# Kernel optimization log

Measured on AMD Instinct MI355X. Metric: run time of the kernel, lower is better.

Reference implementation:

```python
import jax, jax.numpy as jnp
import numpy as np
from jax import lax

B, C, H, W = 32, 3, 256, 256
P, D, E, K = 16, 256, 8, 2
HP, WP = H // P, W // P
N = HP * WP
GATE_IN = C * P * P  # 768
GATE_HID = D // 2    # 128


def _mk(key, shape, scale=0.02):
    return scale * jax.random.normal(key, shape, dtype=jnp.float32)


def setup_inputs() -> dict:
    key = jax.random.key(0)
    ks = jax.random.split(key, 20)
    inp = {
        "x": jax.random.normal(ks[0], (B, C, H, W), dtype=jnp.float32),
        # gate MLP: Linear(768,128) -> ReLU -> Linear(128,8)
        "g_w1": _mk(ks[1], (GATE_HID, GATE_IN)),
        "g_b1": jnp.zeros((GATE_HID,), jnp.float32),
        "g_w2": _mk(ks[2], (E, GATE_HID)),
        "g_b2": jnp.zeros((E,), jnp.float32),
        # per-expert CNN params, stacked with leading expert dim E
        "dw1_w": _mk(ks[3], (E, 3, 1, 3, 3)),   "dw1_b": jnp.zeros((E, 3), jnp.float32),
        "pw1_w": _mk(ks[4], (E, 64, 3, 1, 1)),  "pw1_b": jnp.zeros((E, 64), jnp.float32),
        "dw2_w": _mk(ks[5], (E, 64, 1, 3, 3)),  "dw2_b": jnp.zeros((E, 64), jnp.float32),
        "pw2_w": _mk(ks[6], (E, 128, 64, 1, 1)), "pw2_b": jnp.zeros((E, 128), jnp.float32),
        "dw3_w": _mk(ks[7], (E, 128, 1, 3, 3)), "dw3_b": jnp.zeros((E, 128), jnp.float32),
        "pw3_w": _mk(ks[8], (E, D, 128, 1, 1)), "pw3_b": jnp.zeros((E, D), jnp.float32),
    }
    return inp


def _dwconv(x, w, b, stride):
    # depthwise 3x3, padding 1; x: [n, c, h, w]; w: [c, 1, 3, 3]
    c = x.shape[1]
    y = lax.conv_general_dilated(
        x, w, (stride, stride), ((1, 1), (1, 1)),
        dimension_numbers=("NCHW", "OIHW", "NCHW"), feature_group_count=c)
    return jax.nn.relu(y + b[None, :, None, None])


def _pwconv(x, w, b):
    # pointwise 1x1 conv as GEMM; w: [o, c, 1, 1]
    y = jnp.einsum("nchw,oc->nohw", x, w[:, :, 0, 0]) + b[None, :, None, None]
    return jax.nn.relu(y)


def _expert(x, dw1w, dw1b, pw1w, pw1b, dw2w, dw2b, pw2w, pw2b, dw3w, dw3b, pw3w, pw3b):
    # x: [BN, 3, 16, 16] -> [BN, D]
    x = _pwconv(_dwconv(x, dw1w, dw1b, 2), pw1w, pw1b)   # [BN, 64, 8, 8]
    x = _pwconv(_dwconv(x, dw2w, dw2b, 2), pw2w, pw2b)   # [BN, 128, 4, 4]
    x = _pwconv(_dwconv(x, dw3w, dw3b, 2), pw3w, pw3b)   # [BN, 256, 2, 2]
    return x.mean(axis=(2, 3))                            # adaptive avg pool to 1x1


def reference(x, g_w1, g_b1, g_w2, g_b2,
              dw1_w, dw1_b, pw1_w, pw1_b, dw2_w, dw2_b, pw2_w, pw2_b,
              dw3_w, dw3_b, pw3_w, pw3_b):
    b = x.shape[0]
    # nn.Unfold(kernel=P, stride=P): columns ordered (c, di, dj)
    patches = x.reshape(b, C, HP, P, WP, P).transpose(0, 2, 4, 1, 3, 5)  # [B,hp,wp,C,P,P]
    patches_sp = patches.reshape(b * N, C, P, P)
    patches_flat = patches_sp.reshape(b * N, GATE_IN)

    # gate (eval mode: dropout is identity)
    h = jax.nn.relu(patches_flat @ g_w1.T + g_b1)
    logits = h @ g_w2.T + g_b2                       # [BN, E]
    topk_vals, topk_idx = lax.top_k(logits, K)       # [BN, K]
    weights = jax.nn.softmax(topk_vals, axis=-1)
    one_hot = jax.nn.one_hot(topk_idx, E, dtype=x.dtype)   # [BN, K, E]
    routing = (one_hot * weights[..., None]).sum(axis=1)   # [BN, E]

    # run all experts densely (as the original does), then combine
    expert_outs = jax.vmap(_expert, in_axes=(None,) + (0,) * 12)(
        patches_sp, dw1_w, dw1_b, pw1_w, pw1_b, dw2_w, dw2_b,
        pw2_w, pw2_b, dw3_w, dw3_b, pw3_w, pw3_b)   # [E, BN, D]
    out = jnp.einsum("ne,end->nd", routing, expert_outs)  # [BN, D]

    features = out.reshape(b, HP, WP, D).transpose(0, 3, 1, 2)  # [B, D, hp, wp]
    load_balance_loss = jnp.float32(0.0)  # eval mode
    return features, load_balance_loss
```

## Files before the change

### kernel.cpp

```cpp
#include <hip/hip_runtime.h>

#define BN 8192
#define GIN 768

#define O_ROUTE_I 0UL
#define O_ROUTE_W (O_ROUTE_I + (size_t)BN*2*4)
#define O_COUNTS  (O_ROUTE_W + (size_t)BN*2*4)
#define O_LISTS   (O_COUNTS + 256)
#define O_PW2T    (O_LISTS + (size_t)8*BN*4)
#define O_PW3T    (O_PW2T + (size_t)8*64*128*4)
#define O_SLOT    (O_PW3T + (size_t)8*128*256*4)

__global__ __launch_bounds__(256) void k0_prep(const float* __restrict__ pw2w,
                                               const float* __restrict__ pw3w,
                                               float* __restrict__ pw2t,
                                               float* __restrict__ pw3t,
                                               int* __restrict__ counts)
{
    int tid = blockIdx.x * 256 + threadIdx.x;
    if (tid < 8) counts[tid] = 0;
    for (int idx = tid; idx < 8 * 128 * 64; idx += 256 * 256) {
        int e = idx >> 13; int r = idx & 8191; int oc = r >> 6; int c = r & 63;
        pw2t[(size_t)e * 8192 + c * 128 + oc] = pw2w[idx];
    }
    for (int idx = tid; idx < 8 * 256 * 128; idx += 256 * 256) {
        int e = idx >> 15; int r = idx & 32767; int oc = r >> 7; int c = r & 127;
        pw3t[(size_t)e * 32768 + c * 256 + oc] = pw3w[idx];
    }
}

__global__ __launch_bounds__(256) void k1_gate(
    const float* __restrict__ x, const float* __restrict__ w1,
    const float* __restrict__ b1, const float* __restrict__ w2,
    const float* __restrict__ b2,
    int* __restrict__ route_i, float* __restrict__ route_w,
    int* __restrict__ counts, int* __restrict__ lists)
{
    __shared__ __align__(16) float A[32][44];
    __shared__ __align__(16) float Wl[32][132];
    __shared__ float hl[32][132];
    __shared__ float ll[32][8];

    int tid = threadIdx.x;
    int pblk = blockIdx.x * 32;

    int pgrp = tid & 7;
    int hgrp = tid >> 3;
    float acc[4][4] = {};

    int sp  = tid >> 3;
    int sk4 = (tid & 7) * 4;
    int swh = tid >> 1;
    int swk = (tid & 1) * 16;

    int patchA = pblk + sp;
    int bA = patchA >> 8; int nA = patchA & 255; int hpA = nA >> 4; int wpA = nA & 15;

    for (int kc = 0; kc < GIN; kc += 32) {
        {
            int k = kc + sk4;
            int c = k >> 8; int rem = k & 255; int ri = rem >> 4; int j = rem & 15;
            const float* src = x + (((size_t)(bA * 3 + c) * 256 + hpA * 16 + ri) * 256 + wpA * 16 + j);
            float4 a4 = *reinterpret_cast<const float4*>(src);
            A[sk4 + 0][sp] = a4.x; A[sk4 + 1][sp] = a4.y;
            A[sk4 + 2][sp] = a4.z; A[sk4 + 3][sp] = a4.w;
        }
        {
            const float* wsrc = w1 + (size_t)swh * GIN + kc + swk;
            #pragma unroll
            for (int q = 0; q < 4; q++) {
                float4 w4 = *reinterpret_cast<const float4*>(wsrc + q * 4);
                Wl[swk + q * 4 + 0][swh] = w4.x; Wl[swk + q * 4 + 1][swh] = w4.y;
                Wl[swk + q * 4 + 2][swh] = w4.z; Wl[swk + q * 4 + 3][swh] = w4.w;
            }
        }
        __syncthreads();
        float cacc[4][4] = {};
        #pragma unroll
        for (int k2 = 0; k2 < 32; k2++) {
            float4 av = *reinterpret_cast<const float4*>(&A[k2][pgrp * 4]);
            float4 wv = *reinterpret_cast<const float4*>(&Wl[k2][hgrp * 4]);
            float aa[4] = {av.x, av.y, av.z, av.w};
            float ww[4] = {wv.x, wv.y, wv.z, wv.w};
            #pragma unroll
            for (int i = 0; i < 4; i++) {
                #pragma unroll
                for (int jj = 0; jj < 4; jj++) cacc[i][jj] += aa[i] * ww[jj];
            }
        }
        #pragma unroll
        for (int i = 0; i < 4; i++) {
            #pragma unroll
            for (int jj = 0; jj < 4; jj++) acc[i][jj] += cacc[i][jj];
        }
        __syncthreads();
    }

    #pragma unroll
    for (int jj = 0; jj < 4; jj++) {
        float bb = b1[hgrp * 4 + jj];
        #pragma unroll
        for (int i = 0; i < 4; i++) {
            float v = acc[i][jj] + bb;
            hl[pgrp * 4 + i][hgrp * 4 + jj] = v > 0.f ? v : 0.f;
        }
    }
    __syncthreads();

    {
        int lp = tid >> 3; int le = tid & 7;
        float lacc = b2[le];
        const float* wrow = w2 + le * 128;
        for (int h = 0; h < 128; h++) lacc += hl[lp][h] * wrow[h];
        ll[lp][le] = lacc;
    }
    __syncthreads();

    if (tid < 32) {
        int patch = pblk + tid;
        float v[8];
        #pragma unroll
        for (int e = 0; e < 8; e++) v[e] = ll[tid][e];
        int e0 = 0; float m0 = v[0];
        #pragma unroll
        for (int e = 1; e < 8; e++) if (v[e] > m0) { m0 = v[e]; e0 = e; }
        int e1 = -1; float m1 = -3.0e38f;
        #pragma unroll
        for (int e = 0; e < 8; e++) if (e != e0 && v[e] > m1) { m1 = v[e]; e1 = e; }
        float t = expf(m1 - m0);
        float w0 = 1.f / (1.f + t);
        float w1v = t * w0;
        route_i[patch * 2] = e0; route_i[patch * 2 + 1] = e1;
        route_w[patch * 2] = w0; route_w[patch * 2 + 1] = w1v;
        int p0 = atomicAdd(&counts[e0], 1);
        lists[e0 * BN + p0] = patch * 2;
        int p1 = atomicAdd(&counts[e1], 1);
        lists[e1 * BN + p1] = patch * 2 + 1;
    }
}

__global__ __launch_bounds__(256, 3) void k23_expert(
    const float* __restrict__ x, const int* __restrict__ counts,
    const int* __restrict__ lists,
    const float* __restrict__ dw1w, const float* __restrict__ dw1b,
    const float* __restrict__ pw1w, const float* __restrict__ pw1b,
    const float* __restrict__ dw2w, const float* __restrict__ dw2b,
    const float* __restrict__ pw2t, const float* __restrict__ pw2b,
    const float* __restrict__ dw3w, const float* __restrict__ dw3b,
    const float* __restrict__ pw3t, const float* __restrict__ pw3b,
    float* __restrict__ slot)
{
    __shared__ __align__(16) float buf1[4][2176];
    __shared__ __align__(16) float buf2[4][1088];
    __shared__ int psl[4];

    int e = blockIdx.x & 7;
    int chunk = blockIdx.x >> 3;
    int cnt = counts[e];
    int base = chunk * 4;
    if (base >= cnt) return;
    int n_en = cnt - base; if (n_en > 4) n_en = 4;
    int tid = threadIdx.x;
    if (tid < 4) psl[tid] = (tid < n_en) ? lists[e * BN + base + tid] : 0;
    __syncthreads();

    int en = tid >> 6; int l = tid & 63;
    bool act = en < n_en;
    int pslot = psl[en];
    int patch = pslot >> 1;
    int b = patch >> 8, nn = patch & 255, hp = nn >> 4, wp = nn & 15;

    float* pl  = buf1[en];
    float* d1  = buf1[en] + 1024;
    float* p2  = buf1[en];
    float* d2t = buf2[en];
    float* d3  = buf2[en];

    if (act) {
        int r = l >> 2; int j4 = (l & 3) * 4;
        #pragma unroll
        for (int c = 0; c < 3; c++) {
            const float* src = x + (((size_t)(b * 3 + c) * 256 + hp * 16 + r) * 256 + wp * 16 + j4);
            float4 v = *reinterpret_cast<const float4*>(src);
            *reinterpret_cast<float4*>(&pl[c * 320 + r * 20 + j4]) = v;
        }
    }
    __syncthreads();

    if (act) {
        int oh = l >> 3, ow = l & 7;
        #pragma unroll
        for (int c = 0; c < 3; c++) {
            const float* w9 = dw1w + (e * 3 + c) * 9;
            float acc = dw1b[e * 3 + c];
            #pragma unroll
            for (int ki = 0; ki < 3; ki++) {
                int ih = oh * 2 - 1 + ki;
                if ((unsigned)ih < 16u) {
                    #pragma unroll
                    for (int kj = 0; kj < 3; kj++) {
                        int iw = ow * 2 - 1 + kj;
                        if ((unsigned)iw < 16u) acc += pl[c * 320 + ih * 20 + iw] * w9[ki * 3 + kj];
                    }
                }
            }
            d1[c * 64 + l] = acc > 0.f ? acc : 0.f;
        }
    }
    __syncthreads();

    if (act) {
        const float* w3 = pw1w + (e * 64 + l) * 3;
        float pw0 = w3[0], pw1v = w3[1], pw2v = w3[2];
        float pb = pw1b[e * 64 + l];
        float p1r[64];
        #pragma unroll
        for (int p4 = 0; p4 < 16; p4++) {
            float4 a0 = *reinterpret_cast<const float4*>(&d1[0 * 64 + p4 * 4]);
            float4 a1 = *reinterpret_cast<const float4*>(&d1[1 * 64 + p4 * 4]);
            float4 a2 = *reinterpret_cast<const float4*>(&d1[2 * 64 + p4 * 4]);
            float v0 = pb + a0.x * pw0 + a1.x * pw1v + a2.x * pw2v;
            float v1 = pb + a0.y * pw0 + a1.y * pw1v + a2.y * pw2v;
            float v2 = pb + a0.z * pw0 + a1.z * pw1v + a2.z * pw2v;
            float v3 = pb + a0.w * pw0 + a1.w * pw1v + a2.w * pw2v;
            p1r[p4 * 4 + 0] = v0 > 0.f ? v0 : 0.f;
            p1r[p4 * 4 + 1] = v1 > 0.f ? v1 : 0.f;
            p1r[p4 * 4 + 2] = v2 > 0.f ? v2 : 0.f;
            p1r[p4 * 4 + 3] = v3 > 0.f ? v3 : 0.f;
        }
        const float* w9 = dw2w + (e * 64 + l) * 9;
        float wd[9];
        #pragma unroll
        for (int i = 0; i < 9; i++) wd[i] = w9[i];
        float bd = dw2b[e * 64 + l];
        #pragma unroll
        for (int pos = 0; pos < 16; pos++) {
            int oh = pos >> 2, ow = pos & 3;
            float acc = bd;
            #pragma unroll
            for (int ki = 0; ki < 3; ki++) {
                int ih = oh * 2 - 1 + ki;
                if ((unsigned)ih < 8u) {
                    #pragma unroll
                    for (int kj = 0; kj < 3; kj++) {
                        int iw = ow * 2 - 1 + kj;
                        if ((unsigned)iw < 8u) acc += p1r[ih * 8 + iw] * wd[ki * 3 + kj];
                    }
                }
            }
            d2t[pos * 68 + l] = acc > 0.f ? acc : 0.f;
        }
    }
    __syncthreads();

    {
        int ocg = l & 15; int pq = l >> 4;
        int oc0 = ocg * 8; int p0 = pq * 4;
        if (act) {
            float acc[8][4] = {};
            const float* wbase = pw2t + (size_t)e * 8192;
            for (int c4 = 0; c4 < 16; c4++) {
                float4 a0 = *reinterpret_cast<const float4*>(&d2t[(p0 + 0) * 68 + c4 * 4]);
                float4 a1 = *reinterpret_cast<const float4*>(&d2t[(p0 + 1) * 68 + c4 * 4]);
                float4 a2 = *reinterpret_cast<const float4*>(&d2t[(p0 + 2) * 68 + c4 * 4]);
                float4 a3 = *reinterpret_cast<const float4*>(&d2t[(p0 + 3) * 68 + c4 * 4]);
                float av[4][4] = {{a0.x, a1.x, a2.x, a3.x}, {a0.y, a1.y, a2.y, a3.y},
                                  {a0.z, a1.z, a2.z, a3.z}, {a0.w, a1.w, a2.w, a3.w}};
                #pragma unroll
                for (int cc = 0; cc < 4; cc++) {
                    int c = c4 * 4 + cc;
                    float4 wa = *reinterpret_cast<const float4*>(wbase + c * 128 + oc0);
                    float4 wb = *reinterpret_cast<const float4*>(wbase + c * 128 + oc0 + 4);
                    float wv[8] = {wa.x, wa.y, wa.z, wa.w, wb.x, wb.y, wb.z, wb.w};
                    #pragma unroll
                    for (int j = 0; j < 8; j++) {
                        #pragma unroll
                        for (int i = 0; i < 4; i++) acc[j][i] += wv[j] * av[cc][i];
                    }
                }
            }
            #pragma unroll
            for (int j = 0; j < 8; j++) {
                float bb = pw2b[e * 128 + oc0 + j];
                #pragma unroll
                for (int i = 0; i < 4; i++) {
                    float v = acc[j][i] + bb;
                    p2[(oc0 + j) * 17 + p0 + i] = v > 0.f ? v : 0.f;
                }
            }
        }
    }
    __syncthreads();

    if (act) {
        #pragma unroll
        for (int chb = 0; chb < 128; chb += 64) {
            int ch = chb + l;
            const float* w9 = dw3w + (e * 128 + ch) * 9;
            float bb = dw3b[e * 128 + ch];
            #pragma unroll
            for (int pos = 0; pos < 4; pos++) {
                int oh = pos >> 1, ow = pos & 1;
                float acc = bb;
                #pragma unroll
                for (int ki = 0; ki < 3; ki++) {
                    int ih = oh * 2 - 1 + ki;
                    if ((unsigned)ih < 4u) {
                        #pragma unroll
                        for (int kj = 0; kj < 3; kj++) {
                            int iw = ow * 2 - 1 + kj;
                            if ((unsigned)iw < 4u) acc += p2[ch * 17 + ih * 4 + iw] * w9[ki * 3 + kj];
                        }
                    }
                }
                d3[ch * 4 + pos] = acc > 0.f ? acc : 0.f;
            }
        }
    }
    __syncthreads();

    if (act) {
        int oc0 = l * 4;
        const float* wbase = pw3t + (size_t)e * 32768;
        float acc[4][4] = {};
        for (int c = 0; c < 128; c++) {
            float4 a = *reinterpret_cast<const float4*>(&d3[c * 4]);
            float4 w = *reinterpret_cast<const float4*>(wbase + c * 256 + oc0);
            float av[4] = {a.x, a.y, a.z, a.w};
            float wv[4] = {w.x, w.y, w.z, w.w};
            #pragma unroll
            for (int j = 0; j < 4; j++) {
                #pragma unroll
                for (int i = 0; i < 4; i++) acc[j][i] += wv[j] * av[i];
            }
        }
        float o4[4];
        #pragma unroll
        for (int j = 0; j < 4; j++) {
            float bb = pw3b[e * 256 + oc0 + j];
            float s = 0.f;
            #pragma unroll
            for (int i = 0; i < 4; i++) {
                float v = acc[j][i] + bb;
                s += (v > 0.f ? v : 0.f);
            }
            o4[j] = 0.25f * s;
        }
        *reinterpret_cast<float4*>(slot + (size_t)pslot * 256 + oc0) =
            make_float4(o4[0], o4[1], o4[2], o4[3]);
    }
}

__global__ __launch_bounds__(256) void k4_comb(
    const float* __restrict__ slot, const float* __restrict__ route_w,
    float* __restrict__ out)
{
    __shared__ float cl[16][257];
    int bx = blockIdx.x;
    int b = bx >> 4; int hp = bx & 15;
    int tid = threadIdx.x;
    int d = tid;
    for (int wp = 0; wp < 16; wp++) {
        int n = (b * 16 + hp) * 16 + wp;
        float w0 = route_w[n * 2], w1 = route_w[n * 2 + 1];
        float v = w0 * slot[(size_t)(n * 2) * 256 + d] + w1 * slot[(size_t)(n * 2 + 1) * 256 + d];
        cl[wp][d] = v;
    }
    __syncthreads();
    int wp = tid & 15; int dg = tid >> 4;
    for (int r = 0; r < 16; r++) {
        int dd = r * 16 + dg;
        out[(((size_t)b * 256 + dd) * 16 + hp) * 16 + wp] = cl[wp][dd];
    }
    if (bx == 0 && tid == 0) out[(size_t)BN * 256] = 0.0f;
}

extern "C" void kernel_launch(void* const* d_in, const int* in_sizes, int n_in,
                              void* d_out, int out_size, void* d_ws, size_t ws_size,
                              hipStream_t stream)
{
    const float* x    = (const float*)d_in[0];
    const float* gw1  = (const float*)d_in[1];
    const float* gb1  = (const float*)d_in[2];
    const float* gw2  = (const float*)d_in[3];
    const float* gb2  = (const float*)d_in[4];
    const float* dw1w = (const float*)d_in[5];
    const float* dw1b = (const float*)d_in[6];
    const float* pw1w = (const float*)d_in[7];
    const float* pw1b = (const float*)d_in[8];
    const float* dw2w = (const float*)d_in[9];
    const float* dw2b = (const float*)d_in[10];
    const float* pw2w = (const float*)d_in[11];
    const float* pw2b = (const float*)d_in[12];
    const float* dw3w = (const float*)d_in[13];
    const float* dw3b = (const float*)d_in[14];
    const float* pw3w = (const float*)d_in[15];
    const float* pw3b = (const float*)d_in[16];

    char* ws = (char*)d_ws;
    int*   route_i = (int*)(ws + O_ROUTE_I);
    float* route_w = (float*)(ws + O_ROUTE_W);
    int*   counts  = (int*)(ws + O_COUNTS);
    int*   lists   = (int*)(ws + O_LISTS);
    float* pw2t    = (float*)(ws + O_PW2T);
    float* pw3t    = (float*)(ws + O_PW3T);
    float* slot    = (float*)(ws + O_SLOT);
    float* out     = (float*)d_out;

    hipLaunchKernelGGL(k0_prep, dim3(256), dim3(256), 0, stream,
                       pw2w, pw3w, pw2t, pw3t, counts);
    hipLaunchKernelGGL(k1_gate, dim3(BN / 32), dim3(256), 0, stream,
                       x, gw1, gb1, gw2, gb2, route_i, route_w, counts, lists);
    hipLaunchKernelGGL(k23_expert, dim3(8 * 2048), dim3(256), 0, stream,
                       x, counts, lists, dw1w, dw1b, pw1w, pw1b, dw2w, dw2b,
                       pw2t, pw2b, dw3w, dw3b, pw3t, pw3b, slot);
    hipLaunchKernelGGL(k4_comb, dim3(512), dim3(256), 0, stream,
                       slot, route_w, out);
}
```

Measured before the change: 550.0 us.

## Make expert kernel wave-synchronous, shrink LDS, swizzle pw2 output layout

Each 64-lane wave already owns one routed patch, so every block-wide __syncthreads is removed. Inactive waves now exit early instead of being masked, and the patch slot is read straight from the list rather than staged through shared memory. The two shared buffers merge into one smaller per-wave buffer with re-planned aliasing, and launch bounds rise from 3 to 4 blocks per SM. The pw2 output drops its 17-float row padding for a 16-stride XOR-style rotated layout to avoid bank conflicts. This relies on implicit wave-level ordering of LDS accesses with no barrier or fence, which the compiler does not guarantee.

Measured after the change: 578.6 us. 5.2% more time.

```diff
diff --git a/kernel.cpp b/kernel.cpp
--- a/kernel.cpp
+++ b/kernel.cpp
@@ -139,7 +139,7 @@
     }
 }
 
-__global__ __launch_bounds__(256, 3) void k23_expert(
+__global__ __launch_bounds__(256, 4) void k23_expert(
     const float* __restrict__ x, const int* __restrict__ counts,
     const int* __restrict__ lists,
     const float* __restrict__ dw1w, const float* __restrict__ dw1b,
@@ -150,33 +150,27 @@
     const float* __restrict__ pw3t, const float* __restrict__ pw3b,
     float* __restrict__ slot)
 {
-    __shared__ __align__(16) float buf1[4][2176];
-    __shared__ __align__(16) float buf2[4][1088];
-    __shared__ int psl[4];
+    __shared__ __align__(16) float buf[4][2560];
 
     int e = blockIdx.x & 7;
     int chunk = blockIdx.x >> 3;
     int cnt = counts[e];
     int base = chunk * 4;
     if (base >= cnt) return;
-    int n_en = cnt - base; if (n_en > 4) n_en = 4;
     int tid = threadIdx.x;
-    if (tid < 4) psl[tid] = (tid < n_en) ? lists[e * BN + base + tid] : 0;
-    __syncthreads();
-
     int en = tid >> 6; int l = tid & 63;
-    bool act = en < n_en;
-    int pslot = psl[en];
+    if (base + en >= cnt) return;
+    int pslot = lists[e * BN + base + en];
     int patch = pslot >> 1;
     int b = patch >> 8, nn = patch & 255, hp = nn >> 4, wp = nn & 15;
 
-    float* pl  = buf1[en];
-    float* d1  = buf1[en] + 1024;
-    float* p2  = buf1[en];
-    float* d2t = buf2[en];
-    float* d3  = buf2[en];
-
-    if (act) {
+    float* pl  = buf[en];
+    float* d1  = buf[en] + 2048;
+    float* d2t = buf[en];
+    float* p2  = buf[en];
+    float* d3  = buf[en] + 2048;
+
+    {
         int r = l >> 2; int j4 = (l & 3) * 4;
         #pragma unroll
         for (int c = 0; c < 3; c++) {
@@ -185,9 +179,8 @@
             *reinterpret_cast<float4*>(&pl[c * 320 + r * 20 + j4]) = v;
         }
     }
-    __syncthreads();
-
-    if (act) {
+
+    {
         int oh = l >> 3, ow = l & 7;
         #pragma unroll
         for (int c = 0; c < 3; c++) {
@@ -207,9 +200,8 @@
             d1[c * 64 + l] = acc > 0.f ? acc : 0.f;
         }
     }
-    __syncthreads();
-
-    if (act) {
+
+    {
         const float* w3 = pw1w + (e * 64 + l) * 3;
         float pw0 = w3[0], pw1v = w3[1], pw2v = w3[2];
         float pb = pw1b[e * 64 + l];
@@ -251,51 +243,48 @@
             d2t[pos * 68 + l] = acc > 0.f ? acc : 0.f;
         }
     }
-    __syncthreads();
 
     {
         int ocg = l & 15; int pq = l >> 4;
         int oc0 = ocg * 8; int p0 = pq * 4;
-        if (act) {
-            float acc[8][4] = {};
-            const float* wbase = pw2t + (size_t)e * 8192;
-            for (int c4 = 0; c4 < 16; c4++) {
-                float4 a0 = *reinterpret_cast<const float4*>(&d2t[(p0 + 0) * 68 + c4 * 4]);
-                float4 a1 = *reinterpret_cast<const float4*>(&d2t[(p0 + 1) * 68 + c4 * 4]);
-                float4 a2 = *reinterpret_cast<const float4*>(&d2t[(p0 + 2) * 68 + c4 * 4]);
-                float4 a3 = *reinterpret_cast<const float4*>(&d2t[(p0 + 3) * 68 + c4 * 4]);
-                float av[4][4] = {{a0.x, a1.x, a2.x, a3.x}, {a0.y, a1.y, a2.y, a3.y},
-                                  {a0.z, a1.z, a2.z, a3.z}, {a0.w, a1.w, a2.w, a3.w}};
+        float acc[8][4] = {};
+        const float* wbase = pw2t + (size_t)e * 8192;
+        for (int c4 = 0; c4 < 16; c4++) {
+            float4 a0 = *reinterpret_cast<const float4*>(&d2t[(p0 + 0) * 68 + c4 * 4]);
+            float4 a1 = *reinterpret_cast<const float4*>(&d2t[(p0 + 1) * 68 + c4 * 4]);
+            float4 a2 = *reinterpret_cast<const float4*>(&d2t[(p0 + 2) * 68 + c4 * 4]);
+            float4 a3 = *reinterpret_cast<const float4*>(&d2t[(p0 + 3) * 68 + c4 * 4]);
+            float av[4][4] = {{a0.x, a1.x, a2.x, a3.x}, {a0.y, a1.y, a2.y, a3.y},
+                              {a0.z, a1.z, a2.z, a3.z}, {a0.w, a1.w, a2.w, a3.w}};
+            #pragma unroll
+            for (int cc = 0; cc < 4; cc++) {
+                int c = c4 * 4 + cc;
+                float4 wa = *reinterpret_cast<const float4*>(wbase + c * 128 + oc0);
+                float4 wb = *reinterpret_cast<const float4*>(wbase + c * 128 + oc0 + 4);
+                float wv[8] = {wa.x, wa.y, wa.z, wa.w, wb.x, wb.y, wb.z, wb.w};
                 #pragma unroll
-                for (int cc = 0; cc < 4; cc++) {
-                    int c = c4 * 4 + cc;
-                    float4 wa = *reinterpret_cast<const float4*>(wbase + c * 128 + oc0);
-                    float4 wb = *reinterpret_cast<const float4*>(wbase + c * 128 + oc0 + 4);
-                    float wv[8] = {wa.x, wa.y, wa.z, wa.w, wb.x, wb.y, wb.z, wb.w};
+                for (int j = 0; j < 8; j++) {
                     #pragma unroll
-                    for (int j = 0; j < 8; j++) {
-                        #pragma unroll
-                        for (int i = 0; i < 4; i++) acc[j][i] += wv[j] * av[cc][i];
-                    }
+                    for (int i = 0; i < 4; i++) acc[j][i] += wv[j] * av[cc][i];
                 }
             }
-            #pragma unroll
-            for (int j = 0; j < 8; j++) {
-                float bb = pw2b[e * 128 + oc0 + j];
-                #pragma unroll
-                for (int i = 0; i < 4; i++) {
-                    float v = acc[j][i] + bb;
-                    p2[(oc0 + j) * 17 + p0 + i] = v > 0.f ? v : 0.f;
-                }
-            }
-        }
-    }
-    __syncthreads();
-
-    if (act) {
+        }
+        #pragma unroll
+        for (int j = 0; j < 8; j++) {
+            float bb = pw2b[e * 128 + oc0 + j];
+            #pragma unroll
+            for (int i = 0; i < 4; i++) {
+                float v = acc[j][i] + bb;
+                p2[(oc0 + j) * 16 + ((p0 + i + ocg) & 15)] = v > 0.f ? v : 0.f;
+            }
+        }
+    }
+
+    {
         #pragma unroll
         for (int chb = 0; chb < 128; chb += 64) {
             int ch = chb + l;
+            int grp = ch >> 3;
             const float* w9 = dw3w + (e * 128 + ch) * 9;
             float bb = dw3b[e * 128 + ch];
             #pragma unroll
@@ -309,7 +298,8 @@
                         #pragma unroll
                         for (int kj = 0; kj < 3; kj++) {
                             int iw = ow * 2 - 1 + kj;
-                            if ((unsigned)iw < 4u) acc += p2[ch * 17 + ih * 4 + iw] * w9[ki * 3 + kj];
+                            if ((unsigned)iw < 4u)
+                                acc += p2[ch * 16 + ((ih * 4 + iw + grp) & 15)] * w9[ki * 3 + kj];
                         }
                     }
                 }
@@ -317,9 +307,8 @@
             }
         }
     }
-    __syncthreads();
-
-    if (act) {
+
+    {
         int oc0 = l * 4;
         const float* wbase = pw3t + (size_t)e * 32768;
         float acc[4][4] = {};
```
